# Kernel tuning notes

Hardware: AMD Instinct MI355X
Metric: run time of the kernel (lower is better)

## Reference

```python
import jax, jax.numpy as jnp
import numpy as np

D_MODEL = 1024
D_STATE = 128
D_CONV = 4
EXPAND = 2
HEADDIM = 64
NGROUPS = 1
CHUNK = 256
D_INNER = EXPAND * D_MODEL          # 2048
NHEADS = D_INNER // HEADDIM         # 32
D_IN_PROJ = 2 * D_INNER + 2 * NGROUPS * D_STATE + NHEADS  # 4384
CONV_DIM = D_INNER + 2 * NGROUPS * D_STATE                # 2304
BATCH, SEQLEN = 2, 2048


def rmsnorm(x, w, eps=1e-6):
    ms = jnp.mean(x * x, axis=-1, keepdims=True)
    return w * (x * jax.lax.rsqrt(ms + eps))


def layernorm(x, eps=1e-5):
    mu = jnp.mean(x, axis=-1, keepdims=True)
    var = jnp.mean((x - mu) ** 2, axis=-1, keepdims=True)
    return (x - mu) * jax.lax.rsqrt(var + eps)


def activation_quant(x):
    # int8-style fake quant with STE, scale differentiable (matches torch)
    amax = jnp.clip(jnp.max(jnp.abs(x), axis=-1, keepdims=True), 1e-5, None)
    scale = 127.0 / amax
    q = jnp.clip(jnp.round(x * scale), -128, 127)
    return (jax.lax.stop_gradient(q - x * scale) + x * scale) / scale


def weight_quant(w):
    # ternary {-1,0,1}; note: NOT rescaled by scale (matches the triton kernel)
    scale = jnp.clip(jnp.mean(jnp.abs(w)), 1e-5, None)
    wq = jnp.clip(jnp.round(w / scale), -1.0, 1.0)
    return w + jax.lax.stop_gradient(wq - w)  # STE: identity grad


def bitlinear(x, w):
    return activation_quant(layernorm(x)) @ weight_quant(w).T


def segsum(x):
    # x: [..., T] -> [..., T, T] lower-triangular cumulative segment sums
    T = x.shape[-1]
    cs = jnp.cumsum(x, axis=-1)
    ss = cs[..., :, None] - cs[..., None, :]
    mask = jnp.tril(jnp.ones((T, T), dtype=bool))
    return jnp.where(mask, ss, -jnp.inf)


def ssd(u, a, B, C, chunk):
    # u: b l h p (= x*dt); a: b l h (= A*dt); B, C: b l h n (per-head)
    b, l, h, p = u.shape
    n = B.shape[-1]
    c = l // chunk
    u = u.reshape(b, c, chunk, h, p)
    a = a.reshape(b, c, chunk, h).transpose(0, 3, 1, 2)   # b h c s
    B = B.reshape(b, c, chunk, h, n)
    C = C.reshape(b, c, chunk, h, n)
    a_cs = jnp.cumsum(a, axis=-1)                          # b h c s
    L = jnp.exp(segsum(a))                                 # b h c s s
    Y_diag = jnp.einsum('bclhn,bcshn,bhcls,bcshp->bclhp', C, B, L, u)
    decay_states = jnp.exp(a_cs[..., -1:] - a_cs)          # b h c s
    states = jnp.einsum('bclhn,bhcl,bclhp->bchpn', B, decay_states, u)
    a_chunk = jnp.pad(a_cs[..., -1], ((0, 0), (0, 0), (1, 0)))  # b h (c+1)
    decay_chunk = jnp.exp(segsum(a_chunk))                 # b h (c+1) (c+1)
    states = jnp.concatenate([jnp.zeros_like(states[:, :1]), states], axis=1)
    new_states = jnp.einsum('bhzc,bchpn->bzhpn', decay_chunk, states)
    prev_states = new_states[:, :-1]                       # state entering each chunk
    Y_off = jnp.einsum('bclhn,bchpn,bhcl->bclhp', C, prev_states, jnp.exp(a_cs))
    return (Y_diag + Y_off).reshape(b, l, h, p)


def setup_inputs() -> dict:
    key = jax.random.key(0)
    ks = jax.random.split(key, 6)
    hidden_states = jax.random.normal(ks[0], (BATCH, SEQLEN, D_MODEL), jnp.float32)
    in_proj_w = jax.random.normal(ks[1], (D_IN_PROJ, D_MODEL), jnp.float32) / np.sqrt(D_MODEL).astype(np.float32)
    out_proj_w = jax.random.normal(ks[2], (D_MODEL, D_INNER), jnp.float32) / np.sqrt(D_INNER).astype(np.float32)
    conv_w = jax.random.normal(ks[3], (CONV_DIM, D_CONV), jnp.float32) * 0.1
    conv_b = jnp.zeros((CONV_DIM,), jnp.float32)
    A_log = jnp.log(jnp.arange(1, NHEADS + 1, dtype=jnp.float32))
    Dp = jnp.ones((NHEADS,), jnp.float32)
    dt_min, dt_max, dt_floor = 1e-3, 1e-1, 1e-4
    inv_dt = jnp.exp(jax.random.uniform(ks[4], (NHEADS,)) * (np.log(dt_max) - np.log(dt_min)) + np.log(dt_min))
    inv_dt = jnp.clip(inv_dt, dt_floor, None)
    dt_bias = inv_dt + jnp.log(-jnp.expm1(-inv_dt))
    norm_w = jnp.ones((D_MODEL,), jnp.float32)
    out_norm_w = jnp.ones((D_INNER,), jnp.float32)
    return dict(hidden_states=hidden_states, norm_w=norm_w, in_proj_w=in_proj_w,
                conv_w=conv_w, conv_b=conv_b, A_log=A_log, Dp=Dp, dt_bias=dt_bias,
                out_norm_w=out_norm_w, out_proj_w=out_proj_w)


def reference(hidden_states, norm_w, in_proj_w, conv_w, conv_b, A_log, Dp, dt_bias, out_norm_w, out_proj_w):
    b, l, _ = hidden_states.shape
    h = rmsnorm(hidden_states, norm_w)
    zxbcdt = bitlinear(h, in_proj_w)                       # b l (2*d_inner + 2*g*n + h)
    z = zxbcdt[..., :D_INNER]
    xBC = zxbcdt[..., D_INNER:D_INNER + CONV_DIM]
    dt = zxbcdt[..., D_INNER + CONV_DIM:]                  # b l h
    # causal depthwise conv1d (kernel D_CONV) + silu
    xp = jnp.pad(xBC, ((0, 0), (D_CONV - 1, 0), (0, 0)))
    conv = sum(xp[:, k:k + l, :] * conv_w[:, k] for k in range(D_CONV)) + conv_b
    xBC = jax.nn.silu(conv)
    x = xBC[..., :D_INNER].reshape(b, l, NHEADS, HEADDIM)
    Bm = xBC[..., D_INNER:D_INNER + NGROUPS * D_STATE].reshape(b, l, NGROUPS, D_STATE)
    Cm = xBC[..., D_INNER + NGROUPS * D_STATE:].reshape(b, l, NGROUPS, D_STATE)
    hpg = NHEADS // NGROUPS
    Bh = jnp.repeat(Bm, hpg, axis=2)                       # b l h n
    Ch = jnp.repeat(Cm, hpg, axis=2)
    dt = jax.nn.softplus(dt + dt_bias)                     # dt_softplus=True
    A = -jnp.exp(A_log)
    y = ssd(x * dt[..., None], dt * A, Bh, Ch, CHUNK)      # b l h p
    y = y + x * Dp[None, None, :, None]                    # D skip
    y = y * jax.nn.silu(z).reshape(b, l, NHEADS, HEADDIM)  # z gate
    y = rmsnorm(y.reshape(b, l, D_INNER), out_norm_w)
    out = bitlinear(y, out_proj_w)
    return hidden_states + out
```

## Files before the change

kernel.cpp:

```cpp
#include <hip/hip_runtime.h>
#include <stdint.h>
#include <stddef.h>
#include <math.h>

#define TOKS 4096
#define DM   1024
#define DIP  4384
#define DI   2048
#define CVD  2304
#define NH   32
#define HD   64
#define DST  128
#define NCH  8
#define CHK  256

typedef int v4i  __attribute__((ext_vector_type(4)));
typedef int v16i __attribute__((ext_vector_type(16)));
typedef short s8v __attribute__((ext_vector_type(8)));
typedef float f16v __attribute__((ext_vector_type(16)));
typedef unsigned short ushort_t;

static const size_t OFF_ZX    = 0;
static const size_t OFF_SX    = OFF_ZX + (size_t)TOKS*DIP*4;
static const size_t OFF_ST    = OFF_SX + (size_t)TOKS*CVD*4;
static const size_t OFF_YG    = OFF_ST + (size_t)2*NCH*NH*HD*DST*4;
static const size_t OFF_Q1    = OFF_YG + (size_t)TOKS*DI*4;
static const size_t OFF_Q2    = OFF_Q1 + (size_t)TOKS*DM;
static const size_t OFF_WQ1   = OFF_Q2 + (size_t)TOKS*DI;
static const size_t OFF_WQ2   = OFF_WQ1 + (size_t)DIP*DM;
static const size_t OFF_RS1   = OFF_WQ2 + (size_t)DM*DI;
static const size_t OFF_RS2   = OFF_RS1 + (size_t)TOKS*4;
static const size_t OFF_DT    = OFF_RS2 + (size_t)TOKS*4;
static const size_t OFF_ACS   = OFF_DT + (size_t)TOKS*NH*4;
static const size_t OFF_CSUM  = OFF_ACS + (size_t)512*CHK*8;
static const size_t OFF_PART  = OFF_CSUM + 512*8;
static const size_t OFF_WSC   = OFF_PART + 1024*8;

__device__ __forceinline__ ushort_t f2bf(float x) {
  union { float f; unsigned int u; } v; v.f = x;
  unsigned int r = v.u + 0x7FFFu + ((v.u >> 16) & 1u);
  return (ushort_t)(r >> 16);
}
__device__ __forceinline__ float bf2f(ushort_t h) {
  union { unsigned int u; float f; } v; v.u = ((unsigned int)h) << 16;
  return v.f;
}
__device__ __forceinline__ void splitfrag(float4 a, float4 b, s8v& hi, s8v& lo) {
  union { s8v v; ushort_t e[8]; } H, L;
  float f[8] = {a.x, a.y, a.z, a.w, b.x, b.y, b.z, b.w};
#pragma unroll
  for (int i = 0; i < 8; i++) {
    ushort_t h = f2bf(f[i]);
    H.e[i] = h;
    L.e[i] = f2bf(f[i] - bf2f(h));
  }
  hi = H.v; lo = L.v;
}

__device__ __forceinline__ double bsumd(double v, double* sb) {
#pragma unroll
  for (int o = 32; o; o >>= 1) v += __shfl_down(v, o);
  int lane = threadIdx.x & 63, w = threadIdx.x >> 6;
  __syncthreads();
  if (lane == 0) sb[w] = v;
  __syncthreads();
  return sb[0] + sb[1] + sb[2] + sb[3];
}
__device__ __forceinline__ double bmaxd(double v, double* sb) {
#pragma unroll
  for (int o = 32; o; o >>= 1) v = fmax(v, __shfl_down(v, o));
  int lane = threadIdx.x & 63, w = threadIdx.x >> 6;
  __syncthreads();
  if (lane == 0) sb[w] = v;
  __syncthreads();
  return fmax(fmax(sb[0], sb[1]), fmax(sb[2], sb[3]));
}

__global__ void __launch_bounds__(256) k_absmean(const float* __restrict__ w, int n, double* __restrict__ part) {
  double s = 0.0;
  for (int i = blockIdx.x * 256 + threadIdx.x; i < n; i += 512 * 256) s += (double)fabsf(w[i]);
  __shared__ double sb[4];
  s = bsumd(s, sb);
  if (threadIdx.x == 0) part[blockIdx.x] = s;
}

__global__ void __launch_bounds__(256) k_wscale(const double* __restrict__ part, double* __restrict__ wsc, int n1, int n2) {
  __shared__ double sb[4];
  double s = part[threadIdx.x] + part[threadIdx.x + 256];
  double t1 = bsumd(s, sb);
  __syncthreads();
  s = part[512 + threadIdx.x] + part[512 + threadIdx.x + 256];
  double t2 = bsumd(s, sb);
  if (threadIdx.x == 0) {
    wsc[0] = fmax(t1 / (double)n1, 1e-5);
    wsc[1] = fmax(t2 / (double)n2, 1e-5);
  }
}

__global__ void __launch_bounds__(256) k_tern(const float* __restrict__ w, int n, const double* __restrict__ wsc, int which, int8_t* __restrict__ out) {
  int i = blockIdx.x * 256 + threadIdx.x;
  if (i < n) {
    double sc = wsc[which];
    double q = fmin(fmax(rint((double)w[i] / sc), -1.0), 1.0);
    out[i] = (int8_t)q;
  }
}

template <int D>
__global__ void __launch_bounds__(256) k_normquant(const float* __restrict__ in, const float* __restrict__ w,
// ... 56 lines not shown
      int4 bv;
      if (n0 + row < N) bv = *(const int4*)(W + (size_t)(n0 + row) * K + k0 + kc);
      else { bv.x = bv.y = bv.z = bv.w = 0; }
      *(int4*)(Bl + row * 80 + kc) = bv;
    }
    __syncthreads();
#pragma unroll
    for (int ks = 0; ks < 2; ++ks) {
      v4i af[2], bf[2];
#pragma unroll
      for (int tm = 0; tm < 2; ++tm)
        af[tm] = *(const v4i*)(Al + (wm * 64 + tm * 32 + l31) * 80 + ks * 32 + lh * 16);
#pragma unroll
      for (int tn = 0; tn < 2; ++tn)
        bf[tn] = *(const v4i*)(Bl + (wn * 64 + tn * 32 + l31) * 80 + ks * 32 + lh * 16);
#pragma unroll
      for (int tm = 0; tm < 2; ++tm)
#pragma unroll
        for (int tn = 0; tn < 2; ++tn)
          acc[tm][tn] = __builtin_amdgcn_mfma_i32_32x32x32_i8(af[tm], bf[tn], acc[tm][tn], 0, 0, 0);
    }
  }

#pragma unroll
  for (int tm = 0; tm < 2; ++tm)
#pragma unroll
    for (int tn = 0; tn < 2; ++tn) {
      int n = n0 + wn * 64 + tn * 32 + l31;
      if (n < N) {
#pragma unroll
        for (int r = 0; r < 16; ++r) {
          int mrel = (r & 3) + 8 * (r >> 2) + 4 * lh;
          int m = m0 + wm * 64 + tm * 32 + mrel;
          float v = rs[m] * (float)acc[tm][tn][r];
          if (addend) v += addend[(size_t)m * N + n];
          out[(size_t)m * N + n] = v;
        }
      }
    }
}

__global__ void __launch_bounds__(256) k_conv(const float* __restrict__ zx, const float* __restrict__ cw,
                                              const float* __restrict__ cb, float* __restrict__ sx) {
  int c = blockIdx.x * 256 + threadIdx.x;
  int t = blockIdx.y;
  int b = t >> 11, l = t & 2047;
  float acc = cb[c];
#pragma unroll
  for (int k = 0; k < 4; k++) {
    int li = l - 3 + k;
    if (li >= 0) acc = fmaf(zx[(size_t)(b * 2048 + li) * DIP + DI + c], cw[c * 4 + k], acc);
  }
  sx[(size_t)t * CVD + c] = acc / (1.f + expf(-acc));
}

__global__ void __launch_bounds__(256) k_dt(const float* __restrict__ zx, const float* __restrict__ dt_bias,
                                            float* __restrict__ dtv) {
  int idx = blockIdx.x * 256 + threadIdx.x;
  int t = idx >> 5, h = idx & 31;
  float x = zx[(size_t)t * DIP + (DI + CVD) + h] + dt_bias[h];
  dtv[idx] = fmaxf(x, 0.f) + log1pf(expf(-fabsf(x)));
}

__global__ void __launch_bounds__(256) k_cumsum(const float* __restrict__ dtv, const float* __restrict__ A_log,
                                                double* __restrict__ acs, double* __restrict__ csum) {
  int bid = blockIdx.x;
  int h = bid & 31, bc = bid >> 5;
  int s = threadIdx.x;
  int tok = bc * 256 + s;
  double negA = -exp((double)A_log[h]);
  double a = (double)dtv[tok * 32 + h] * negA;
  __shared__ double buf[256];
  buf[s] = a;
  __syncthreads();
  for (int o = 1; o < 256; o <<= 1) {
    double add = (s >= o) ? buf[s - o] : 0.0;
    __syncthreads();
    buf[s] += add;
    __syncthreads();
  }
  acs[(size_t)bid * 256 + s] = buf[s];
  if (s == 255) csum[bid] = buf[s];
}

__global__ void __launch_bounds__(256, 4) k_states2(const float* __restrict__ sx, const float* __restrict__ dtv,
                                                    const double* __restrict__ acs, const double* __restrict__ csum,
                                                    float* __restrict__ states) {
  int r = blockIdx.x;
  int h = r & 31, bc = r >> 5;
  int t = threadIdx.x, tx = t & 15, ty = t >> 4;
  __shared__ float du[64 * 68];
  double last = csum[r];
  float acc[4][8] = {};
  for (int s0 = 0; s0 < 256; s0 += 64) {
    __syncthreads();
    {
      int s = t >> 2, pg = (t & 3) * 16;
      int tok = bc * 256 + s0 + s;
      float w = expf((float)(last - acs[(size_t)r * 256 + s0 + s])) * dtv[(size_t)tok * 32 + h];
      const float* xr = sx + (size_t)tok * CVD + h * 64 + pg;
      float* dst = &du[s * 68 + pg];
#pragma unroll
      for (int i = 0; i < 4; i++) {
        float4 v = *(const float4*)(xr + i * 4);
        v.x *= w; v.y *= w; v.z *= w; v.w *= w;
        *(float4*)(dst + i * 4) = v;
      }
    }
    __syncthreads();
#pragma unroll 4
    for (int s = 0; s < 64; s++) {
      int tok = bc * 256 + s0 + s;
      const float* br = sx + (size_t)tok * CVD + DI + ty * 8;
      float4 b0 = *(const float4*)(br);
      float4 b1 = *(const float4*)(br + 4);
      float4 d4 = *(const float4*)(&du[s * 68 + tx * 4]);
      float dd[4] = {d4.x, d4.y, d4.z, d4.w};
      float bv[8] = {b0.x, b0.y, b0.z, b0.w, b1.x, b1.y, b1.z, b1.w};
#pragma unroll
      for (int i = 0; i < 4; i++)
#pragma unroll
        for (int j = 0; j < 8; j++) acc[i][j] = fmaf(dd[i], bv[j], acc[i][j]);
    }
  }
  size_t base = (size_t)r * (HD * DST);
#pragma unroll
  for (int i = 0; i < 4; i++) {
    float4 v0, v1;
    v0.x = acc[i][0]; v0.y = acc[i][1]; v0.z = acc[i][2]; v0.w = acc[i][3];
    v1.x = acc[i][4]; v1.y = acc[i][5]; v1.z = acc[i][6]; v1.w = acc[i][7];
    *(float4*)(states + base + (size_t)(tx * 4 + i) * DST + ty * 8) = v0;
    *(float4*)(states + base + (size_t)(tx * 4 + i) * DST + ty * 8 + 4) = v1;
  }
}

__global__ void __launch_bounds__(256) k_chunkscan(float* __restrict__ states, const double* __restrict__ csum) {
  int idx = blockIdx.x * 256 + threadIdx.x;
  int n = idx & 127, p = (idx >> 7) & 63, h = (idx >> 13) & 31, b = idx >> 18;
  float Nv = 0.f;
  for (int c = 0; c < 8; c++) {
    int bid = (b * 8 + c) * 32 + h;
    size_t addr = (size_t)bid * (HD * DST) + p * DST + n;
    float s = states[addr];
    states[addr] = Nv;
    Nv = Nv * expf((float)csum[bid]) + s;
  }
}

__global__ void __launch_bounds__(256, 2) k_y4(const float* __restrict__ sx, const float* __restrict__ dtv,
                                               const double* __restrict__ acs, const float* __restrict__ prev,
                                               const float* __restrict__ zx, const float* __restrict__ Dp,
                                               float* __restrict__ yg) {
  int bid = blockIdx.x;
  int r = bid >> 1, half = bid & 1;
  int h = r & 31, bc = r >> 5;
  int t = threadIdx.x;
  int w = t >> 6, lane = t & 63;
  int l31 = lane & 31, lhf = lane >> 5;
  int lw = half * 128 + w * 32;

  __shared__ ushort_t Bh[32 * 136], Blo[32 * 136];
  __shared__ ushort_t Uh[64 * 40],  Ulo[64 * 40];
  __shared__ float    Sll[4][32 * 36];
  __shared__ double   acs_s[256];

  acs_s[t] = acs[(size_t)r * 256 + t];
  __syncthreads();

  s8v Ch[8], Cl[8];
  {
    int tokl = bc * 256 + lw + l31;
    const float* Crow = sx + (size_t)tokl * CVD + DI + DST;
#pragma unroll
    for (int ks = 0; ks < 8; ++ks) {
      float4 a = *(const float4*)(Crow + ks * 16 + lhf * 8);
      float4 b = *(const float4*)(Crow + ks * 16 + lhf * 8 + 4);
      splitfrag(a, b, Ch[ks], Cl[ks]);
    }
  }

  f16v Yacc[2] = {};
#pragma unroll
  for (int pt = 0; pt < 2; ++pt) {
    const float* pr = prev + (size_t)r * (HD * DST) + (size_t)(pt * 32 + l31) * DST;
#pragma unroll
    for (int ks = 0; ks < 8; ++ks) {
      float4 a = *(const float4*)(pr + ks * 16 + lhf * 8);
      float4 b = *(const float4*)(pr + ks * 16 + lhf * 8 + 4);
      s8v ph, pl;
      splitfrag(a, b, ph, pl);
      Yacc[pt] = __builtin_amdgcn_mfma_f32_32x32x16_bf16(Ch[ks], ph, Yacc[pt], 0, 0, 0);
      Yacc[pt] = __builtin_amdgcn_mfma_f32_32x32x16_bf16(Ch[ks], pl, Yacc[pt], 0, 0, 0);
      Yacc[pt] = __builtin_amdgcn_mfma_f32_32x32x16_bf16(Cl[ks], ph, Yacc[pt], 0, 0, 0);
    }
  }
#pragma unroll
  for (int rr = 0; rr < 16; ++rr) {
    int lrow = (rr & 3) + 8 * (rr >> 2) + 4 * lhf;
    float el = expf((float)acs_s[lw + lrow]);
    Yacc[0][rr] *= el;
    Yacc[1][rr] *= el;
  }

  int nsub = half * 4 + 4;
  for (int st = 0; st < nsub; ++st) {
    int s0 = st * 32;
    __syncthreads();
    {
      int srow = t >> 3, n0 = (t & 7) * 16;
      const float* src = sx + (size_t)(bc * 256 + s0 + srow) * CVD + DI + n0;
      float f[16];
#pragma unroll
      for (int i = 0; i < 4; i++) {
        float4 v = *(const float4*)(src + i * 4);
        f[i * 4 + 0] = v.x; f[i * 4 + 1] = v.y; f[i * 4 + 2] = v.z; f[i * 4 + 3] = v.w;
      }
#pragma unroll
      for (int j = 0; j < 8; j++) {
        ushort_t h0 = f2bf(f[2 * j]), h1 = f2bf(f[2 * j + 1]);
        ushort_t l0 = f2bf(f[2 * j] - bf2f(h0)), l1 = f2bf(f[2 * j + 1] - bf2f(h1));
        *(unsigned int*)(&Bh[srow * 136 + n0 + 2 * j])  = (unsigned int)h0 | ((unsigned int)h1 << 16);
        *(unsigned int*)(&Blo[srow * 136 + n0 + 2 * j]) = (unsigned int)l0 | ((unsigned int)l1 << 16);
      }
    }
    {
      int srow = t >> 3, p0 = (t & 7) * 8;
      const float* xr = sx + (size_t)(bc * 256 + s0 + srow) * CVD + h * 64 + p0;
      float4 v0 = *(const float4*)(xr);
      float4 v1 = *(const float4*)(xr + 4);
      float f[8] = {v0.x, v0.y, v0.z, v0.w, v1.x, v1.y, v1.z, v1.w};
#pragma unroll
      for (int j = 0; j < 8; j++) {
        ushort_t hh = f2bf(f[j]);
        Uh[(p0 + j) * 40 + srow] = hh;
        Ulo[(p0 + j) * 40 + srow] = f2bf(f[j] - bf2f(hh));
      }
    }
    __syncthreads();

    if (s0 <= lw + 31) {
      f16v Sacc = {};
#pragma unroll
      for (int ks = 0; ks < 8; ++ks) {
        s8v bh = *(const s8v*)(&Bh[l31 * 136 + ks * 16 + lhf * 8]);
        s8v bl = *(const s8v*)(&Blo[l31 * 136 + ks * 16 + lhf * 8]);
        Sacc = __builtin_amdgcn_mfma_f32_32x32x16_bf16(Ch[ks], bh, Sacc, 0, 0, 0);
        Sacc = __builtin_amdgcn_mfma_f32_32x32x16_bf16(Ch[ks], bl, Sacc, 0, 0, 0);
        Sacc = __builtin_amdgcn_mfma_f32_32x32x16_bf16(Cl[ks], bh, Sacc, 0, 0, 0);
      }
      int sg = s0 + l31;
      float dts = dtv[(size_t)(bc * 256 + sg) * 32 + h];
      double a_s = acs_s[sg];
#pragma unroll
      for (int rr = 0; rr < 16; ++rr) {
        int lrow = (rr & 3) + 8 * (rr >> 2) + 4 * lhf;
        int lg = lw + lrow;
        float v = 0.f;
        if (sg <= lg) v = expf((float)(acs_s[lg] - a_s)) * Sacc[rr] * dts;
        Sll[w][lrow * 36 + l31] = v;
      }
#pragma unroll
      for (int ks2 = 0; ks2 < 2; ++ks2) {
        float4 a = *(const float4*)(&Sll[w][l31 * 36 + ks2 * 16 + lhf * 8]);
        float4 b = *(const float4*)(&Sll[w][l31 * 36 + ks2 * 16 + lhf * 8 + 4]);
        s8v sah, sal;
        splitfrag(a, b, sah, sal);
#pragma unroll
        for (int pt = 0; pt < 2; ++pt) {
          s8v uh = *(const s8v*)(&Uh[(pt * 32 + l31) * 40 + ks2 * 16 + lhf * 8]);
          s8v ul = *(const s8v*)(&Ulo[(pt * 32 + l31) * 40 + ks2 * 16 + lhf * 8]);
          Yacc[pt] = __builtin_amdgcn_mfma_f32_32x32x16_bf16(sah, uh, Yacc[pt], 0, 0, 0);
          Yacc[pt] = __builtin_amdgcn_mfma_f32_32x32x16_bf16(sah, ul, Yacc[pt], 0, 0, 0);
          Yacc[pt] = __builtin_amdgcn_mfma_f32_32x32x16_bf16(sal, uh, Yacc[pt], 0, 0, 0);
        }
      }
    }
  }

  float dph = Dp[h];
#pragma unroll
  for (int pt = 0; pt < 2; ++pt) {
    int p = pt * 32 + l31;
#pragma unroll
    for (int rr = 0; rr < 16; ++rr) {
      int lrow = (rr & 3) + 8 * (rr >> 2) + 4 * lhf;
      size_t tok = (size_t)(bc * 256 + lw + lrow);
      float xv = sx[tok * CVD + h * 64 + p];
      float zv = zx[tok * DIP + h * 64 + p];
      float y = (Yacc[pt][rr] + xv * dph) * (zv / (1.f + expf(-zv)));
      yg[tok * DI + h * 64 + p] = y;
    }
  }
}

extern "C" void kernel_launch(void* const* d_in, const int* in_sizes, int n_in,
                              void* d_out, int out_size, void* d_ws, size_t ws_size,
                              hipStream_t stream) {
  const float* hidden   = (const float*)d_in[0];
  const float* norm_w   = (const float*)d_in[1];
  const float* in_proj  = (const float*)d_in[2];
  const float* conv_w   = (const float*)d_in[3];
  const float* conv_b   = (const float*)d_in[4];
  const float* A_log    = (const float*)d_in[5];
  const float* Dp       = (const float*)d_in[6];
  const float* dt_bias  = (const float*)d_in[7];
  const float* out_norm = (const float*)d_in[8];
  const float* out_proj = (const float*)d_in[9];
  float* out = (float*)d_out;

  char* ws = (char*)d_ws;
  float*  zx    = (float*)(ws + OFF_ZX);
  float*  sx    = (float*)(ws + OFF_SX);
  float*  st    = (float*)(ws + OFF_ST);
  float*  yg    = (float*)(ws + OFF_YG);
  int8_t* q1    = (int8_t*)(ws + OFF_Q1);
  int8_t* q2    = (int8_t*)(ws + OFF_Q2);
  int8_t* wq1   = (int8_t*)(ws + OFF_WQ1);
  int8_t* wq2   = (int8_t*)(ws + OFF_WQ2);
  float*  rs1   = (float*)(ws + OFF_RS1);
  float*  rs2   = (float*)(ws + OFF_RS2);
  float*  dtv   = (float*)(ws + OFF_DT);
  double* acs   = (double*)(ws + OFF_ACS);
  double* csum  = (double*)(ws + OFF_CSUM);
  double* part  = (double*)(ws + OFF_PART);
  double* wsc   = (double*)(ws + OFF_WSC);

  const int n1 = DIP * DM, n2 = DM * DI;

  hipLaunchKernelGGL(k_absmean, dim3(512), dim3(256), 0, stream, in_proj, n1, part);
  hipLaunchKernelGGL(k_absmean, dim3(512), dim3(256), 0, stream, out_proj, n2, part + 512);
  hipLaunchKernelGGL(k_wscale, dim3(1), dim3(256), 0, stream, part, wsc, n1, n2);
  hipLaunchKernelGGL(k_tern, dim3((n1 + 255) / 256), dim3(256), 0, stream, in_proj, n1, wsc, 0, wq1);
  hipLaunchKernelGGL(k_tern, dim3((n2 + 255) / 256), dim3(256), 0, stream, out_proj, n2, wsc, 1, wq2);
  hipLaunchKernelGGL(k_normquant<DM>, dim3(TOKS), dim3(256), 0, stream, hidden, norm_w, q1, rs1);
  hipLaunchKernelGGL(k_gemm_mfma, dim3(TOKS / 128, (DIP + 127) / 128), dim3(256), 0, stream,
                     q1, wq1, rs1, (const float*)nullptr, zx, TOKS, DIP, DM);
  hipLaunchKernelGGL(k_conv, dim3(CVD / 256, TOKS), dim3(256), 0, stream, zx, conv_w, conv_b, sx);
  hipLaunchKernelGGL(k_dt, dim3(TOKS * NH / 256), dim3(256), 0, stream, zx, dt_bias, dtv);
  hipLaunchKernelGGL(k_cumsum, dim3(512), dim3(256), 0, stream, dtv, A_log, acs, csum);
  hipLaunchKernelGGL(k_states2, dim3(512), dim3(256), 0, stream, sx, dtv, acs, csum, st);
  hipLaunchKernelGGL(k_chunkscan, dim3(2 * NH * HD * DST / 256), dim3(256), 0, stream, st, csum);
  hipLaunchKernelGGL(k_y4, dim3(1024), dim3(256), 0, stream, sx, dtv, acs, st, zx, Dp, yg);
  hipLaunchKernelGGL(k_normquant<DI>, dim3(TOKS), dim3(256), 0, stream, yg, out_norm, q2, rs2);
  hipLaunchKernelGGL(k_gemm_mfma, dim3(TOKS / 128, DM / 128), dim3(256), 0, stream,
                     q2, wq2, rs2, hidden, out, TOKS, DM, DI);
  (void)in_sizes; (void)n_in; (void)out_size; (void)ws_size;
}
```

Before: 363.7 us.

## Precompute bf16 hi/lo split of B once and restage U/S tiles in k_y5

A new kernel splits the shared B matrix into bf16 hi/lo pairs once per token, so the y kernel copies ready-made bf16 data instead of re-splitting B in every block. The U tile now goes through a float staging buffer and is transposed with vectorized writes, and the S tile is split into bf16 hi/lo when it is written to shared memory rather than when it is read back. This removes a lot of repeated conversion work, which was duplicated across heads. In exchange it adds a kernel launch, extra workspace traffic, and an extra __syncthreads per sub-tile.

```diff
diff --git a/kernel.cpp b/kernel.cpp
--- a/kernel.cpp
+++ b/kernel.cpp
@@ -35,6 +35,8 @@
 static const size_t OFF_CSUM  = OFF_ACS + (size_t)512*CHK*8;
 static const size_t OFF_PART  = OFF_CSUM + 512*8;
 static const size_t OFF_WSC   = OFF_PART + 1024*8;
+static const size_t OFF_BH    = OFF_WSC + 64;
+static const size_t OFF_BL    = OFF_BH + (size_t)TOKS*128*2;
 
 __device__ __forceinline__ ushort_t f2bf(float x) {
   union { float f; unsigned int u; } v; v.f = x;
@@ -219,6 +221,22 @@
   sx[(size_t)t * CVD + c] = acc / (1.f + expf(-acc));
 }
 
+__global__ void __launch_bounds__(256) k_splitb(const float* __restrict__ sx, ushort_t* __restrict__ bh,
+                                                ushort_t* __restrict__ bl) {
+  int idx = blockIdx.x * 256 + threadIdx.x;
+  int tok = idx >> 5, c4 = (idx & 31) * 4;
+  float4 v = *(const float4*)(sx + (size_t)tok * CVD + DI + c4);
+  float f[4] = {v.x, v.y, v.z, v.w};
+  ushort_t hh[4], ll[4];
+#pragma unroll
+  for (int j = 0; j < 4; j++) { hh[j] = f2bf(f[j]); ll[j] = f2bf(f[j] - bf2f(hh[j])); }
+  uint2 hv, lv;
+  hv.x = (unsigned)hh[0] | ((unsigned)hh[1] << 16); hv.y = (unsigned)hh[2] | ((unsigned)hh[3] << 16);
+  lv.x = (unsigned)ll[0] | ((unsigned)ll[1] << 16); lv.y = (unsigned)ll[2] | ((unsigned)ll[3] << 16);
+  *(uint2*)(bh + (size_t)tok * 128 + c4) = hv;
+  *(uint2*)(bl + (size_t)tok * 128 + c4) = lv;
+}
+
 __global__ void __launch_bounds__(256) k_dt(const float* __restrict__ zx, const float* __restrict__ dt_bias,
                                             float* __restrict__ dtv) {
   int idx = blockIdx.x * 256 + threadIdx.x;
@@ -312,9 +330,10 @@
   }
 }
 
-__global__ void __launch_bounds__(256, 2) k_y4(const float* __restrict__ sx, const float* __restrict__ dtv,
+__global__ void __launch_bounds__(256, 2) k_y5(const float* __restrict__ sx, const float* __restrict__ dtv,
                                                const double* __restrict__ acs, const float* __restrict__ prev,
                                                const float* __restrict__ zx, const float* __restrict__ Dp,
+                                               const ushort_t* __restrict__ bhg, const ushort_t* __restrict__ blg,
                                                float* __restrict__ yg) {
   int bid = blockIdx.x;
   int r = bid >> 1, half = bid & 1;
@@ -324,9 +343,10 @@
   int l31 = lane & 31, lhf = lane >> 5;
   int lw = half * 128 + w * 32;
 
-  __shared__ ushort_t Bh[32 * 136], Blo[32 * 136];
-  __shared__ ushort_t Uh[64 * 40],  Ulo[64 * 40];
-  __shared__ float    Sll[4][32 * 36];
+  __shared__ ushort_t Bh[32 * 132], Bl[32 * 132];
+  __shared__ float    Xs[32 * 69];
+  __shared__ ushort_t Uh[64 * 36], Ul[64 * 36];
+  __shared__ ushort_t Sh[4][32 * 36], Sl[4][32 * 36];
   __shared__ double   acs_s[256];
 
   acs_s[t] = acs[(size_t)r * 256 + t];
@@ -372,71 +392,92 @@
     int s0 = st * 32;
     __syncthreads();
     {
-      int srow = t >> 3, n0 = (t & 7) * 16;
-      const float* src = sx + (size_t)(bc * 256 + s0 + srow) * CVD + DI + n0;
-      float f[16];
-#pragma unroll
-      for (int i = 0; i < 4; i++) {
-        float4 v = *(const float4*)(src + i * 4);
-        f[i * 4 + 0] = v.x; f[i * 4 + 1] = v.y; f[i * 4 + 2] = v.z; f[i * 4 + 3] = v.w;
-      }
-#pragma unroll
-      for (int j = 0; j < 8; j++) {
-        ushort_t h0 = f2bf(f[2 * j]), h1 = f2bf(f[2 * j + 1]);
-        ushort_t l0 = f2bf(f[2 * j] - bf2f(h0)), l1 = f2bf(f[2 * j + 1] - bf2f(h1));
-        *(unsigned int*)(&Bh[srow * 136 + n0 + 2 * j])  = (unsigned int)h0 | ((unsigned int)h1 << 16);
-        *(unsigned int*)(&Blo[srow * 136 + n0 + 2 * j]) = (unsigned int)l0 | ((unsigned int)l1 << 16);
-      }
+      int row = t >> 3, k = t & 7;
+      size_t gbase = (size_t)(bc * 256 + s0 + row) * 128 + k * 16;
+      const uint2* sh0 = (const uint2*)(bhg + gbase);
+      uint2* dh = (uint2*)(&Bh[row * 132 + k * 16]);
+      dh[0] = sh0[0]; dh[1] = sh0[1]; dh[2] = sh0[2]; dh[3] = sh0[3];
+      const uint2* sl0 = (const uint2*)(blg + gbase);
+      uint2* dl = (uint2*)(&Bl[row * 132 + k * 16]);
+      dl[0] = sl0[0]; dl[1] = sl0[1]; dl[2] = sl0[2]; dl[3] = sl0[3];
     }
     {
-      int srow = t >> 3, p0 = (t & 7) * 8;
-      const float* xr = sx + (size_t)(bc * 256 + s0 + srow) * CVD + h * 64 + p0;
+      int srow = t >> 3, pg = (t & 7) * 8;
+      const float* xr = sx + (size_t)(bc * 256 + s0 + srow) * CVD + h * 64 + pg;
       float4 v0 = *(const float4*)(xr);
       float4 v1 = *(const float4*)(xr + 4);
-      float f[8] = {v0.x, v0.y, v0.z, v0.w, v1.x, v1.y, v1.z, v1.w};
+      float* dst = &Xs[srow * 69 + pg];
+      dst[0] = v0.x; dst[1] = v0.y; dst[2] = v0.z; dst[3] = v0.w;
+      dst[4] = v1.x; dst[5] = v1.y; dst[6] = v1.z; dst[7] = v1.w;
+    }
+    __syncthreads();
+    {
+      int p = t >> 2, sg = (t & 3) * 8;
+      ushort_t hh[8], ll[8];
 #pragma unroll
       for (int j = 0; j < 8; j++) {
-        ushort_t hh = f2bf(f[j]);
-        Uh[(p0 + j) * 40 + srow] = hh;
-        Ulo[(p0 + j) * 40 + srow] = f2bf(f[j] - bf2f(hh));
+        float f = Xs[(sg + j) * 69 + p];
+        hh[j] = f2bf(f);
+        ll[j] = f2bf(f - bf2f(hh[j]));
       }
-    }
-    __syncthreads();
-
-    if (s0 <= lw + 31) {
+      uint2 hv0, hv1, lv0, lv1;
+      hv0.x = (unsigned)hh[0] | ((unsigned)hh[1] << 16); hv0.y = (unsigned)hh[2] | ((unsigned)hh[3] << 16);
+      hv1.x = (unsigned)hh[4] | ((unsigned)hh[5] << 16); hv1.y = (unsigned)hh[6] | ((unsigned)hh[7] << 16);
+      lv0.x = (unsigned)ll[0] | ((unsigned)ll[1] << 16); lv0.y = (unsigned)ll[2] | ((unsigned)ll[3] << 16);
+      lv1.x = (unsigned)ll[4] | ((unsigned)ll[5] << 16); lv1.y = (unsigned)ll[6] | ((unsigned)ll[7] << 16);
+      *(uint2*)(&Uh[p * 36 + sg])     = hv0;
+      *(uint2*)(&Uh[p * 36 + sg + 4]) = hv1;
+      *(uint2*)(&Ul[p * 36 + sg])     = lv0;
+      *(uint2*)(&Ul[p * 36 + sg + 4]) = lv1;
+    }
+
+    bool active = (s0 <= lw + 31);
+    if (active) {
       f16v Sacc = {};
 #pragma unroll
       for (int ks = 0; ks < 8; ++ks) {
-        s8v bh = *(const s8v*)(&Bh[l31 * 136 + ks * 16 + lhf * 8]);
-        s8v bl = *(const s8v*)(&Blo[l31 * 136 + ks * 16 + lhf * 8]);
-        Sacc = __builtin_amdgcn_mfma_f32_32x32x16_bf16(Ch[ks], bh, Sacc, 0, 0, 0);
-        Sacc = __builtin_amdgcn_mfma_f32_32x32x16_bf16(Ch[ks], bl, Sacc, 0, 0, 0);
-        Sacc = __builtin_amdgcn_mfma_f32_32x32x16_bf16(Cl[ks], bh, Sacc, 0, 0, 0);
+        union { s8v v; uint2 d[2]; } bh_, bl_;
+        bh_.d[0] = *(const uint2*)(&Bh[l31 * 132 + ks * 16 + lhf * 8]);
+        bh_.d[1] = *(const uint2*)(&Bh[l31 * 132 + ks * 16 + lhf * 8 + 4]);
+        bl_.d[0] = *(const uint2*)(&Bl[l31 * 132 + ks * 16 + lhf * 8]);
+        bl_.d[1] = *(const uint2*)(&Bl[l31 * 132 + ks * 16 + lhf * 8 + 4]);
+        Sacc = __builtin_amdgcn_mfma_f32_32x32x16_bf16(Ch[ks], bh_.v, Sacc, 0, 0, 0);
+        Sacc = __builtin_amdgcn_mfma_f32_32x32x16_bf16(Ch[ks], bl_.v, Sacc, 0, 0, 0);
+        Sacc = __builtin_amdgcn_mfma_f32_32x32x16_bf16(Cl[ks], bh_.v, Sacc, 0, 0, 0);
       }
-      int sg = s0 + l31;
-      float dts = dtv[(size_t)(bc * 256 + sg) * 32 + h];
-      double a_s = acs_s[sg];
+      int sg2 = s0 + l31;
+      float dts = dtv[(size_t)(bc * 256 + sg2) * 32 + h];
+      double a_s = acs_s[sg2];
 #pragma unroll
       for (int rr = 0; rr < 16; ++rr) {
         int lrow = (rr & 3) + 8 * (rr >> 2) + 4 * lhf;
         int lg = lw + lrow;
         float v = 0.f;
-        if (sg <= lg) v = expf((float)(acs_s[lg] - a_s)) * Sacc[rr] * dts;
-        Sll[w][lrow * 36 + l31] = v;
+        if (sg2 <= lg) v = expf((float)(acs_s[lg] - a_s)) * Sacc[rr] * dts;
+        ushort_t hh = f2bf(v);
+        Sh[w][lrow * 36 + l31] = hh;
+        Sl[w][lrow * 36 + l31] = f2bf(v - bf2f(hh));
       }
+    }
+    __syncthreads();
+    if (active) {
 #pragma unroll
       for (int ks2 = 0; ks2 < 2; ++ks2) {
-        float4 a = *(const float4*)(&Sll[w][l31 * 36 + ks2 * 16 + lhf * 8]);
-        float4 b = *(const float4*)(&Sll[w][l31 * 36 + ks2 * 16 + lhf * 8 + 4]);
-        s8v sah, sal;
-        splitfrag(a, b, sah, sal);
+        union { s8v v; uint2 d[2]; } sah, sal;
+        sah.d[0] = *(const uint2*)(&Sh[w][l31 * 36 + ks2 * 16 + lhf * 8]);
+        sah.d[1] = *(const uint2*)(&Sh[w][l31 * 36 + ks2 * 16 + lhf * 8 + 4]);
+        sal.d[0] = *(const uint2*)(&Sl[w][l31 * 36 + ks2 * 16 + lhf * 8]);
+        sal.d[1] = *(const uint2*)(&Sl[w][l31 * 36 + ks2 * 16 + lhf * 8 + 4]);
 #pragma unroll
         for (int pt = 0; pt < 2; ++pt) {
-          s8v uh = *(const s8v*)(&Uh[(pt * 32 + l31) * 40 + ks2 * 16 + lhf * 8]);
-          s8v ul = *(const s8v*)(&Ulo[(pt * 32 + l31) * 40 + ks2 * 16 + lhf * 8]);
-          Yacc[pt] = __builtin_amdgcn_mfma_f32_32x32x16_bf16(sah, uh, Yacc[pt], 0, 0, 0);
-          Yacc[pt] = __builtin_amdgcn_mfma_f32_32x32x16_bf16(sah, ul, Yacc[pt], 0, 0, 0);
-          Yacc[pt] = __builtin_amdgcn_mfma_f32_32x32x16_bf16(sal, uh, Yacc[pt], 0, 0, 0);
+          union { s8v v; uint2 d[2]; } uh, ul;
+          uh.d[0] = *(const uint2*)(&Uh[(pt * 32 + l31) * 36 + ks2 * 16 + lhf * 8]);
+          uh.d[1] = *(const uint2*)(&Uh[(pt * 32 + l31) * 36 + ks2 * 16 + lhf * 8 + 4]);
+          ul.d[0] = *(const uint2*)(&Ul[(pt * 32 + l31) * 36 + ks2 * 16 + lhf * 8]);
+          ul.d[1] = *(const uint2*)(&Ul[(pt * 32 + l31) * 36 + ks2 * 16 + lhf * 8 + 4]);
+          Yacc[pt] = __builtin_amdgcn_mfma_f32_32x32x16_bf16(sah.v, uh.v, Yacc[pt], 0, 0, 0);
+          Yacc[pt] = __builtin_amdgcn_mfma_f32_32x32x16_bf16(sah.v, ul.v, Yacc[pt], 0, 0, 0);
+          Yacc[pt] = __builtin_amdgcn_mfma_f32_32x32x16_bf16(sal.v, uh.v, Yacc[pt], 0, 0, 0);
         }
       }
     }
@@ -489,6 +530,8 @@
   double* csum  = (double*)(ws + OFF_CSUM);
   double* part  = (double*)(ws + OFF_PART);
   double* wsc   = (double*)(ws + OFF_WSC);
+  ushort_t* bhg = (ushort_t*)(ws + OFF_BH);
+  ushort_t* blg = (ushort_t*)(ws + OFF_BL);
 
   const int n1 = DIP * DM, n2 = DM * DI;
 
@@ -501,11 +544,12 @@
   hipLaunchKernelGGL(k_gemm_mfma, dim3(TOKS / 128, (DIP + 127) / 128), dim3(256), 0, stream,
                      q1, wq1, rs1, (const float*)nullptr, zx, TOKS, DIP, DM);
   hipLaunchKernelGGL(k_conv, dim3(CVD / 256, TOKS), dim3(256), 0, stream, zx, conv_w, conv_b, sx);
+  hipLaunchKernelGGL(k_splitb, dim3(512), dim3(256), 0, stream, sx, bhg, blg);
   hipLaunchKernelGGL(k_dt, dim3(TOKS * NH / 256), dim3(256), 0, stream, zx, dt_bias, dtv);
   hipLaunchKernelGGL(k_cumsum, dim3(512), dim3(256), 0, stream, dtv, A_log, acs, csum);
   hipLaunchKernelGGL(k_states2, dim3(512), dim3(256), 0, stream, sx, dtv, acs, csum, st);
   hipLaunchKernelGGL(k_chunkscan, dim3(2 * NH * HD * DST / 256), dim3(256), 0, stream, st, csum);
-  hipLaunchKernelGGL(k_y4, dim3(1024), dim3(256), 0, stream, sx, dtv, acs, st, zx, Dp, yg);
+  hipLaunchKernelGGL(k_y5, dim3(1024), dim3(256), 0, stream, sx, dtv, acs, st, zx, Dp, bhg, blg, yg);
   hipLaunchKernelGGL(k_normquant<DI>, dim3(TOKS), dim3(256), 0, stream, yg, out_norm, q2, rs2);
   hipLaunchKernelGGL(k_gemm_mfma, dim3(TOKS / 128, DM / 128), dim3(256), 0, stream,
                      q2, wq2, rs2, hidden, out, TOKS, DM, DI);
```

New measurement: 361.0 us. No clear change (-0.7%).

## Precompute shared C·B Gram matrix and pre-split bf16 operands for SSD diagonal blocks

Applied to the files above, without the earlier changes.

With a single group, C·Bᵀ is the same for every head. The per-head intra-chunk score matmul in the y kernel is therefore replaced by one Gram matrix per chunk, computed once in a new kernel and read by all 32 heads. B, C, the dt-scaled x (transposed) and the carried states are also pre-split into bf16 hi/lo arrays by separate kernels, so the y kernel no longer does repeated float-to-bf16 splitting and can double-buffer U tiles from global memory. The cost is several extra launches and extra global traffic for the Gram, U and state buffers in exchange for removing redundant MFMA and conversion work per head.

```diff
diff --git a/kernel.cpp b/kernel.cpp
--- a/kernel.cpp
+++ b/kernel.cpp
@@ -23,7 +23,7 @@
 static const size_t OFF_ZX    = 0;
 static const size_t OFF_SX    = OFF_ZX + (size_t)TOKS*DIP*4;
 static const size_t OFF_ST    = OFF_SX + (size_t)TOKS*CVD*4;
-static const size_t OFF_YG    = OFF_ST + (size_t)2*NCH*NH*HD*DST*4;
+static const size_t OFF_YG    = OFF_ST + (size_t)512*HD*DST*4;
 static const size_t OFF_Q1    = OFF_YG + (size_t)TOKS*DI*4;
 static const size_t OFF_Q2    = OFF_Q1 + (size_t)TOKS*DM;
 static const size_t OFF_WQ1   = OFF_Q2 + (size_t)TOKS*DI;
@@ -35,6 +35,15 @@
 static const size_t OFF_CSUM  = OFF_ACS + (size_t)512*CHK*8;
 static const size_t OFF_PART  = OFF_CSUM + 512*8;
 static const size_t OFF_WSC   = OFF_PART + 1024*8;
+static const size_t OFF_BH    = OFF_WSC + 64;
+static const size_t OFF_BL    = OFF_BH  + (size_t)TOKS*128*2;
+static const size_t OFF_CHG   = OFF_BL  + (size_t)TOKS*128*2;
+static const size_t OFF_CLG   = OFF_CHG + (size_t)TOKS*128*2;
+static const size_t OFF_GRAM  = OFF_CLG + (size_t)TOKS*128*2;
+static const size_t OFF_UTH   = OFF_GRAM + (size_t)16*256*256*4;
+static const size_t OFF_UTL   = OFF_UTH + (size_t)512*64*256*2;
+static const size_t OFF_PH    = OFF_UTL + (size_t)512*64*256*2;
+static const size_t OFF_PL    = OFF_PH  + (size_t)512*64*128*2;
 
 __device__ __forceinline__ ushort_t f2bf(float x) {
   union { float f; unsigned int u; } v; v.f = x;
@@ -44,17 +53,6 @@
 __device__ __forceinline__ float bf2f(ushort_t h) {
   union { unsigned int u; float f; } v; v.u = ((unsigned int)h) << 16;
   return v.f;
-}
-__device__ __forceinline__ void splitfrag(float4 a, float4 b, s8v& hi, s8v& lo) {
-  union { s8v v; ushort_t e[8]; } H, L;
-  float f[8] = {a.x, a.y, a.z, a.w, b.x, b.y, b.z, b.w};
-#pragma unroll
-  for (int i = 0; i < 8; i++) {
-    ushort_t h = f2bf(f[i]);
-    H.e[i] = h;
-    L.e[i] = f2bf(f[i] - bf2f(h));
-  }
-  hi = H.v; lo = L.v;
 }
 
 __device__ __forceinline__ double bsumd(double v, double* sb) {
@@ -217,6 +215,28 @@
     if (li >= 0) acc = fmaf(zx[(size_t)(b * 2048 + li) * DIP + DI + c], cw[c * 4 + k], acc);
   }
   sx[(size_t)t * CVD + c] = acc / (1.f + expf(-acc));
+}
+
+__global__ void __launch_bounds__(256) k_splitbc(const float* __restrict__ sx,
+                                                 ushort_t* __restrict__ bh, ushort_t* __restrict__ bl,
+                                                 ushort_t* __restrict__ ch, ushort_t* __restrict__ cl) {
+  int idx = blockIdx.x * 256 + threadIdx.x;
+  int tok = idx >> 6, c4 = (idx & 63) * 4;
+  float4 v = *(const float4*)(sx + (size_t)tok * CVD + DI + c4);
+  float f[4] = {v.x, v.y, v.z, v.w};
+  ushort_t hh[4], ll[4];
+#pragma unroll
+  for (int j = 0; j < 4; j++) { hh[j] = f2bf(f[j]); ll[j] = f2bf(f[j] - bf2f(hh[j])); }
+  uint2 hv, lv;
+  hv.x = (unsigned)hh[0] | ((unsigned)hh[1] << 16); hv.y = (unsigned)hh[2] | ((unsigned)hh[3] << 16);
+  lv.x = (unsigned)ll[0] | ((unsigned)ll[1] << 16); lv.y = (unsigned)ll[2] | ((unsigned)ll[3] << 16);
+  if (c4 < 128) {
+    *(uint2*)(bh + (size_t)tok * 128 + c4) = hv;
+    *(uint2*)(bl + (size_t)tok * 128 + c4) = lv;
+  } else {
+    *(uint2*)(ch + (size_t)tok * 128 + c4 - 128) = hv;
+    *(uint2*)(cl + (size_t)tok * 128 + c4 - 128) = lv;
+  }
 }
 
 __global__ void __launch_bounds__(256) k_dt(const float* __restrict__ zx, const float* __restrict__ dt_bias,
@@ -248,6 +268,86 @@
   if (s == 255) csum[bid] = buf[s];
 }
 
+__global__ void __launch_bounds__(256) k_gram(const ushort_t* __restrict__ bhg, const ushort_t* __restrict__ blg,
+                                              const ushort_t* __restrict__ chg, const ushort_t* __restrict__ clg,
+                                              float* __restrict__ gram) {
+  int blk = blockIdx.x;
+  int bc = blk >> 3, lt = blk & 7;
+  int t = threadIdx.x;
+  int w = t >> 6, lane = t & 63;
+  int l31 = lane & 31, lhf = lane >> 5;
+  __shared__ float Gl[4][32 * 36];
+
+  s8v ch[8], cl[8];
+  size_t tokA = (size_t)(bc * 256 + lt * 32 + l31) * 128;
+#pragma unroll
+  for (int ks = 0; ks < 8; ++ks) {
+    ch[ks] = *(const s8v*)(chg + tokA + ks * 16 + lhf * 8);
+    cl[ks] = *(const s8v*)(clg + tokA + ks * 16 + lhf * 8);
+  }
+  for (int st = w; st <= lt; st += 4) {
+    size_t tokB = (size_t)(bc * 256 + st * 32 + l31) * 128;
+    f16v acc = {};
+#pragma unroll
+    for (int ks = 0; ks < 8; ++ks) {
+      s8v bh = *(const s8v*)(bhg + tokB + ks * 16 + lhf * 8);
+      s8v bl = *(const s8v*)(blg + tokB + ks * 16 + lhf * 8);
+      acc = __builtin_amdgcn_mfma_f32_32x32x16_bf16(ch[ks], bh, acc, 0, 0, 0);
+      acc = __builtin_amdgcn_mfma_f32_32x32x16_bf16(ch[ks], bl, acc, 0, 0, 0);
+      acc = __builtin_amdgcn_mfma_f32_32x32x16_bf16(cl[ks], bh, acc, 0, 0, 0);
+    }
+#pragma unroll
+    for (int rr = 0; rr < 16; ++rr) {
+      int lrow = (rr & 3) + 8 * (rr >> 2) + 4 * lhf;
+      Gl[w][lrow * 36 + l31] = acc[rr];
+    }
+    int lr = lane >> 1, c0 = (lane & 1) * 16;
+    float* gdst = gram + ((size_t)bc * 256 + lt * 32 + lr) * 256 + st * 32 + c0;
+#pragma unroll
+    for (int i = 0; i < 4; ++i)
+      *(float4*)(gdst + i * 4) = *(const float4*)(&Gl[w][lr * 36 + c0 + i * 4]);
+  }
+}
+
+__global__ void __launch_bounds__(256) k_prepuT(const float* __restrict__ sx, const float* __restrict__ dtv,
+                                                ushort_t* __restrict__ uth, ushort_t* __restrict__ utl) {
+  int r = blockIdx.x;
+  int h = r & 31, bc = r >> 5;
+  int t = threadIdx.x;
+  __shared__ float Xs[64 * 68];
+  __shared__ float dts[64];
+  for (int slab = 0; slab < 4; ++slab) {
+    int s0 = slab * 64;
+    if (slab) __syncthreads();
+    if (t < 64) dts[t] = dtv[(size_t)(bc * 256 + s0 + t) * 32 + h];
+    {
+      int s = t >> 2, pg = (t & 3) * 16;
+      const float* xr = sx + (size_t)(bc * 256 + s0 + s) * CVD + h * 64 + pg;
+      float* dst = &Xs[s * 68 + pg];
+#pragma unroll
+      for (int i = 0; i < 4; ++i)
+        *(float4*)(dst + i * 4) = *(const float4*)(xr + i * 4);
+    }
+    __syncthreads();
+    {
+      int p = t >> 2, sg = (t & 3) * 16;
+      union { int4 q[2]; ushort_t e[16]; } H, L;
+#pragma unroll
+      for (int j = 0; j < 16; ++j) {
+        float f = Xs[(sg + j) * 68 + p] * dts[sg + j];
+        ushort_t hh = f2bf(f);
+        H.e[j] = hh;
+        L.e[j] = f2bf(f - bf2f(hh));
+      }
+      size_t base = ((size_t)r * 64 + p) * 256 + s0 + sg;
+      *(int4*)(uth + base) = H.q[0];
+      *(int4*)(uth + base + 8) = H.q[1];
+      *(int4*)(utl + base) = L.q[0];
+      *(int4*)(utl + base + 8) = L.q[1];
+    }
+  }
+}
+
 __global__ void __launch_bounds__(256, 4) k_states2(const float* __restrict__ sx, const float* __restrict__ dtv,
                                                     const double* __restrict__ acs, const double* __restrict__ csum,
                                                     float* __restrict__ states) {
@@ -299,7 +399,8 @@
   }
 }
 
-__global__ void __launch_bounds__(256) k_chunkscan(float* __restrict__ states, const double* __restrict__ csum) {
+__global__ void __launch_bounds__(256) k_chunkscan(float* __restrict__ states, const double* __restrict__ csum,
+                                                   ushort_t* __restrict__ ph, ushort_t* __restrict__ pl) {
   int idx = blockIdx.x * 256 + threadIdx.x;
   int n = idx & 127, p = (idx >> 7) & 63, h = (idx >> 13) & 31, b = idx >> 18;
   float Nv = 0.f;
@@ -308,14 +409,20 @@
     size_t addr = (size_t)bid * (HD * DST) + p * DST + n;
     float s = states[addr];
     states[addr] = Nv;
+    ushort_t hh = f2bf(Nv);
+    ph[addr] = hh;
+    pl[addr] = f2bf(Nv - bf2f(hh));
     Nv = Nv * expf((float)csum[bid]) + s;
   }
 }
 
-__global__ void __launch_bounds__(256, 2) k_y4(const float* __restrict__ sx, const float* __restrict__ dtv,
-                                               const double* __restrict__ acs, const float* __restrict__ prev,
-                                               const float* __restrict__ zx, const float* __restrict__ Dp,
-                                               float* __restrict__ yg) {
+__global__ void __launch_bounds__(256) k_y6(const float* __restrict__ sx, const double* __restrict__ acs,
+                                            const ushort_t* __restrict__ chg, const ushort_t* __restrict__ clg,
+                                            const ushort_t* __restrict__ prevh, const ushort_t* __restrict__ prevl,
+                                            const float* __restrict__ gram,
+                                            const ushort_t* __restrict__ uth, const ushort_t* __restrict__ utl,
+                                            const float* __restrict__ zx, const float* __restrict__ Dp,
+                                            float* __restrict__ yg) {
   int bid = blockIdx.x;
   int r = bid >> 1, half = bid & 1;
   int h = r & 31, bc = r >> 5;
@@ -323,40 +430,41 @@
   int w = t >> 6, lane = t & 63;
   int l31 = lane & 31, lhf = lane >> 5;
   int lw = half * 128 + w * 32;
-
-  __shared__ ushort_t Bh[32 * 136], Blo[32 * 136];
-  __shared__ ushort_t Uh[64 * 40],  Ulo[64 * 40];
-  __shared__ float    Sll[4][32 * 36];
-  __shared__ double   acs_s[256];
-
+  int lg = lw + l31;
+
+  __shared__ ushort_t Uh[2][64 * 36], Ul[2][64 * 36];
+  __shared__ double acs_s[256];
   acs_s[t] = acs[(size_t)r * 256 + t];
+
+  int nsub = half * 4 + 4;
+  {
+    int p = t >> 2, sg = (t & 3) * 8;
+    size_t gb = ((size_t)r * 64 + p) * 256 + sg;
+    const uint2* s1 = (const uint2*)(uth + gb);
+    uint2* d1 = (uint2*)(&Uh[0][p * 36 + sg]);
+    d1[0] = s1[0]; d1[1] = s1[1];
+    const uint2* s2 = (const uint2*)(utl + gb);
+    uint2* d2 = (uint2*)(&Ul[0][p * 36 + sg]);
+    d2[0] = s2[0]; d2[1] = s2[1];
+  }
   __syncthreads();
 
-  s8v Ch[8], Cl[8];
+  f16v Yacc[2] = {};
   {
-    int tokl = bc * 256 + lw + l31;
-    const float* Crow = sx + (size_t)tokl * CVD + DI + DST;
+    size_t ca = (size_t)(bc * 256 + lg) * 128;
 #pragma unroll
     for (int ks = 0; ks < 8; ++ks) {
-      float4 a = *(const float4*)(Crow + ks * 16 + lhf * 8);
-      float4 b = *(const float4*)(Crow + ks * 16 + lhf * 8 + 4);
-      splitfrag(a, b, Ch[ks], Cl[ks]);
-    }
-  }
-
-  f16v Yacc[2] = {};
-#pragma unroll
-  for (int pt = 0; pt < 2; ++pt) {
-    const float* pr = prev + (size_t)r * (HD * DST) + (size_t)(pt * 32 + l31) * DST;
-#pragma unroll
-    for (int ks = 0; ks < 8; ++ks) {
-      float4 a = *(const float4*)(pr + ks * 16 + lhf * 8);
-      float4 b = *(const float4*)(pr + ks * 16 + lhf * 8 + 4);
-      s8v ph, pl;
-      splitfrag(a, b, ph, pl);
-      Yacc[pt] = __builtin_amdgcn_mfma_f32_32x32x16_bf16(Ch[ks], ph, Yacc[pt], 0, 0, 0);
-      Yacc[pt] = __builtin_amdgcn_mfma_f32_32x32x16_bf16(Ch[ks], pl, Yacc[pt], 0, 0, 0);
-      Yacc[pt] = __builtin_amdgcn_mfma_f32_32x32x16_bf16(Cl[ks], ph, Yacc[pt], 0, 0, 0);
+      s8v ch = *(const s8v*)(chg + ca + ks * 16 + lhf * 8);
+      s8v cl = *(const s8v*)(clg + ca + ks * 16 + lhf * 8);
+#pragma unroll
+      for (int pt = 0; pt < 2; ++pt) {
+        size_t pa = ((size_t)r * 64 + pt * 32 + l31) * 128 + ks * 16 + lhf * 8;
+        s8v ph = *(const s8v*)(prevh + pa);
+        s8v pl = *(const s8v*)(prevl + pa);
+        Yacc[pt] = __builtin_amdgcn_mfma_f32_32x32x16_bf16(ch, ph, Yacc[pt], 0, 0, 0);
+        Yacc[pt] = __builtin_amdgcn_mfma_f32_32x32x16_bf16(ch, pl, Yacc[pt], 0, 0, 0);
+        Yacc[pt] = __builtin_amdgcn_mfma_f32_32x32x16_bf16(cl, ph, Yacc[pt], 0, 0, 0);
+      }
     }
   }
 #pragma unroll
@@ -367,79 +475,53 @@
     Yacc[1][rr] *= el;
   }
 
-  int nsub = half * 4 + 4;
   for (int st = 0; st < nsub; ++st) {
-    int s0 = st * 32;
-    __syncthreads();
-    {
-      int srow = t >> 3, n0 = (t & 7) * 16;
-      const float* src = sx + (size_t)(bc * 256 + s0 + srow) * CVD + DI + n0;
-      float f[16];
-#pragma unroll
-      for (int i = 0; i < 4; i++) {
-        float4 v = *(const float4*)(src + i * 4);
-        f[i * 4 + 0] = v.x; f[i * 4 + 1] = v.y; f[i * 4 + 2] = v.z; f[i * 4 + 3] = v.w;
-      }
-#pragma unroll
-      for (int j = 0; j < 8; j++) {
-        ushort_t h0 = f2bf(f[2 * j]), h1 = f2bf(f[2 * j + 1]);
-        ushort_t l0 = f2bf(f[2 * j] - bf2f(h0)), l1 = f2bf(f[2 * j + 1] - bf2f(h1));
-        *(unsigned int*)(&Bh[srow * 136 + n0 + 2 * j])  = (unsigned int)h0 | ((unsigned int)h1 << 16);
-        *(unsigned int*)(&Blo[srow * 136 + n0 + 2 * j]) = (unsigned int)l0 | ((unsigned int)l1 << 16);
-      }
-    }
-    {
-      int srow = t >> 3, p0 = (t & 7) * 8;
-      const float* xr = sx + (size_t)(bc * 256 + s0 + srow) * CVD + h * 64 + p0;
-      float4 v0 = *(const float4*)(xr);
-      float4 v1 = *(const float4*)(xr + 4);
-      float f[8] = {v0.x, v0.y, v0.z, v0.w, v1.x, v1.y, v1.z, v1.w};
-#pragma unroll
-      for (int j = 0; j < 8; j++) {
-        ushort_t hh = f2bf(f[j]);
-        Uh[(p0 + j) * 40 + srow] = hh;
-        Ulo[(p0 + j) * 40 + srow] = f2bf(f[j] - bf2f(hh));
-      }
-    }
-    __syncthreads();
-
+    int s0 = st * 32, cur = st & 1;
+    if (st + 1 < nsub) {
+      int p = t >> 2, sg = (t & 3) * 8;
+      int nb = cur ^ 1;
+      size_t gb = ((size_t)r * 64 + p) * 256 + s0 + 32 + sg;
+      const uint2* s1 = (const uint2*)(uth + gb);
+      uint2* d1 = (uint2*)(&Uh[nb][p * 36 + sg]);
+      d1[0] = s1[0]; d1[1] = s1[1];
+      const uint2* s2 = (const uint2*)(utl + gb);
+      uint2* d2 = (uint2*)(&Ul[nb][p * 36 + sg]);
+      d2[0] = s2[0]; d2[1] = s2[1];
+    }
     if (s0 <= lw + 31) {
-      f16v Sacc = {};
-#pragma unroll
-      for (int ks = 0; ks < 8; ++ks) {
-        s8v bh = *(const s8v*)(&Bh[l31 * 136 + ks * 16 + lhf * 8]);
-        s8v bl = *(const s8v*)(&Blo[l31 * 136 + ks * 16 + lhf * 8]);
-        Sacc = __builtin_amdgcn_mfma_f32_32x32x16_bf16(Ch[ks], bh, Sacc, 0, 0, 0);
-        Sacc = __builtin_amdgcn_mfma_f32_32x32x16_bf16(Ch[ks], bl, Sacc, 0, 0, 0);
-        Sacc = __builtin_amdgcn_mfma_f32_32x32x16_bf16(Cl[ks], bh, Sacc, 0, 0, 0);
-      }
-      int sg = s0 + l31;
-      float dts = dtv[(size_t)(bc * 256 + sg) * 32 + h];
-      double a_s = acs_s[sg];
-#pragma unroll
-      for (int rr = 0; rr < 16; ++rr) {
-        int lrow = (rr & 3) + 8 * (rr >> 2) + 4 * lhf;
-        int lg = lw + lrow;
-        float v = 0.f;
-        if (sg <= lg) v = expf((float)(acs_s[lg] - a_s)) * Sacc[rr] * dts;
-        Sll[w][lrow * 36 + l31] = v;
-      }
+      double a_l = acs_s[lg];
+      const float* gp = gram + ((size_t)(bc * 256 + lg)) * 256 + s0;
 #pragma unroll
       for (int ks2 = 0; ks2 < 2; ++ks2) {
-        float4 a = *(const float4*)(&Sll[w][l31 * 36 + ks2 * 16 + lhf * 8]);
-        float4 b = *(const float4*)(&Sll[w][l31 * 36 + ks2 * 16 + lhf * 8 + 4]);
-        s8v sah, sal;
-        splitfrag(a, b, sah, sal);
+        int kb = ks2 * 16 + lhf * 8;
+        float4 g0 = *(const float4*)(gp + kb);
+        float4 g1 = *(const float4*)(gp + kb + 4);
+        float gv[8] = {g0.x, g0.y, g0.z, g0.w, g1.x, g1.y, g1.z, g1.w};
+        union { s8v v; ushort_t e[8]; } AH, AL;
+#pragma unroll
+        for (int j = 0; j < 8; ++j) {
+          int s = s0 + kb + j;
+          float v = 0.f;
+          if (s <= lg) v = expf((float)(a_l - acs_s[s])) * gv[j];
+          ushort_t hh = f2bf(v);
+          AH.e[j] = hh;
+          AL.e[j] = f2bf(v - bf2f(hh));
+        }
 #pragma unroll
         for (int pt = 0; pt < 2; ++pt) {
-          s8v uh = *(const s8v*)(&Uh[(pt * 32 + l31) * 40 + ks2 * 16 + lhf * 8]);
-          s8v ul = *(const s8v*)(&Ulo[(pt * 32 + l31) * 40 + ks2 * 16 + lhf * 8]);
-          Yacc[pt] = __builtin_amdgcn_mfma_f32_32x32x16_bf16(sah, uh, Yacc[pt], 0, 0, 0);
-          Yacc[pt] = __builtin_amdgcn_mfma_f32_32x32x16_bf16(sah, ul, Yacc[pt], 0, 0, 0);
-          Yacc[pt] = __builtin_amdgcn_mfma_f32_32x32x16_bf16(sal, uh, Yacc[pt], 0, 0, 0);
+          union { s8v v; uint2 d[2]; } uh, ul;
+          int ub = (pt * 32 + l31) * 36 + kb;
+          uh.d[0] = *(const uint2*)(&Uh[cur][ub]);
+          uh.d[1] = *(const uint2*)(&Uh[cur][ub + 4]);
+          ul.d[0] = *(const uint2*)(&Ul[cur][ub]);
+          ul.d[1] = *(const uint2*)(&Ul[cur][ub + 4]);
+          Yacc[pt] = __builtin_amdgcn_mfma_f32_32x32x16_bf16(AH.v, uh.v, Yacc[pt], 0, 0, 0);
+          Yacc[pt] = __builtin_amdgcn_mfma_f32_32x32x16_bf16(AH.v, ul.v, Yacc[pt], 0, 0, 0);
+          Yacc[pt] = __builtin_amdgcn_mfma_f32_32x32x16_bf16(AL.v, uh.v, Yacc[pt], 0, 0, 0);
         }
       }
     }
+    __syncthreads();
   }
 
   float dph = Dp[h];
@@ -489,6 +571,15 @@
   double* csum  = (double*)(ws + OFF_CSUM);
   double* part  = (double*)(ws + OFF_PART);
   double* wsc   = (double*)(ws + OFF_WSC);
+  ushort_t* bhg = (ushort_t*)(ws + OFF_BH);
+  ushort_t* blg = (ushort_t*)(ws + OFF_BL);
+  ushort_t* chg = (ushort_t*)(ws + OFF_CHG);
+  ushort_t* clg = (ushort_t*)(ws + OFF_CLG);
+  float*  gram  = (float*)(ws + OFF_GRAM);
+  ushort_t* uth = (ushort_t*)(ws + OFF_UTH);
+  ushort_t* utl = (ushort_t*)(ws + OFF_UTL);
+  ushort_t* pvh = (ushort_t*)(ws + OFF_PH);
+  ushort_t* pvl = (ushort_t*)(ws + OFF_PL);
 
   const int n1 = DIP * DM, n2 = DM * DI;
 
@@ -501,11 +592,14 @@
   hipLaunchKernelGGL(k_gemm_mfma, dim3(TOKS / 128, (DIP + 127) / 128), dim3(256), 0, stream,
                      q1, wq1, rs1, (const float*)nullptr, zx, TOKS, DIP, DM);
   hipLaunchKernelGGL(k_conv, dim3(CVD / 256, TOKS), dim3(256), 0, stream, zx, conv_w, conv_b, sx);
+  hipLaunchKernelGGL(k_splitbc, dim3(TOKS * 64 / 256), dim3(256), 0, stream, sx, bhg, blg, chg, clg);
   hipLaunchKernelGGL(k_dt, dim3(TOKS * NH / 256), dim3(256), 0, stream, zx, dt_bias, dtv);
   hipLaunchKernelGGL(k_cumsum, dim3(512), dim3(256), 0, stream, dtv, A_log, acs, csum);
+  hipLaunchKernelGGL(k_gram, dim3(128), dim3(256), 0, stream, bhg, blg, chg, clg, gram);
+  hipLaunchKernelGGL(k_prepuT, dim3(512), dim3(256), 0, stream, sx, dtv, uth, utl);
   hipLaunchKernelGGL(k_states2, dim3(512), dim3(256), 0, stream, sx, dtv, acs, csum, st);
-  hipLaunchKernelGGL(k_chunkscan, dim3(2 * NH * HD * DST / 256), dim3(256), 0, stream, st, csum);
-  hipLaunchKernelGGL(k_y4, dim3(1024), dim3(256), 0, stream, sx, dtv, acs, st, zx, Dp, yg);
+  hipLaunchKernelGGL(k_chunkscan, dim3(2 * NH * HD * DST / 256), dim3(256), 0, stream, st, csum, pvh, pvl);
+  hipLaunchKernelGGL(k_y6, dim3(1024), dim3(256), 0, stream, sx, acs, chg, clg, pvh, pvl, gram, uth, utl, zx, Dp, yg);
   hipLaunchKernelGGL(k_normquant<DI>, dim3(TOKS), dim3(256), 0, stream, yg, out_norm, q2, rs2);
   hipLaunchKernelGGL(k_gemm_mfma, dim3(TOKS / 128, DM / 128), dim3(256), 0, stream,
                      q2, wq2, rs2, hidden, out, TOKS, DM, DI);
```

New measurement: 388.9 us. +6.9%, slower.
